# Kernel optimization log

Measured on AMD Instinct MI355X. Metric: run time of the kernel, lower is better.

## Reference

```python
import jax, jax.numpy as jnp
import numpy as np

# ---- module hyperparameters (init_kwargs) ----
V0 = 1.0
SIGMA0 = 0.5
GAUSS_CONST = V0 / (np.sqrt(2.0 * np.pi) * SIGMA0)
NW, NF, D, H = 4096, 16, 3, 256  # walkers, fermions, dimensions, hidden width
N = NF * D


def setup_inputs() -> dict:
    key = jax.random.key(0)
    k0, k1, k2, k3 = jax.random.split(key, 4)
    sc = lambda k, shape, fan_in: jax.random.normal(k, shape, jnp.float32) / np.sqrt(fan_in).astype(np.float32)
    return {
        "x": jax.random.normal(k0, (NW, NF, D), jnp.float32),
        "W1": sc(k1, (N, H), N),
        "b1": jnp.zeros((H,), jnp.float32),
        "W2": sc(k2, (H, H), H),
        "b2": jnp.zeros((H,), jnp.float32),
        "w3": sc(k3, (H,), H),
        "b3": jnp.zeros((), jnp.float32),
    }


def _logpsi(xf, W1, b1, W2, b2, w3, b3):
    # xf: (N,) flattened single-walker coordinates -> scalar log|psi|
    h = jnp.tanh(xf @ W1 + b1)
    h = jnp.tanh(h @ W2 + b2)
    return h @ w3 + b3


def reference(x, W1, b1, W2, b2, w3, b3):
    nw, nf, d = x.shape
    xflat = x.reshape(nw, nf * d)

    f = lambda xf: _logpsi(xf, W1, b1, W2, b2, w3, b3)
    grad_f = jax.grad(f)

    def kinetic_one(xf):
        g = grad_f(xf)                      # (N,) d logpsi / dx
        hess = jax.jacfwd(grad_f)(xf)       # (N, N) forward-over-reverse Hessian
        lap = jnp.trace(hess)
        return -0.5 * (lap + jnp.sum(g * g))

    kin = jax.vmap(kinetic_one)(xflat)      # (nw,)

    # harmonic potential 1/2 sum x^2
    pot = 0.5 * jnp.sum(xflat * xflat, axis=1)

    # Gaussian interaction, faithful to source: unsqueeze(-2)/unsqueeze(-1) on
    # (nw, nf, d) broadcasts to (nw, nf, d, d) intra-particle coordinate diffs,
    # then sum over last axis -> (nw, nf, d), triu(k=1) over trailing (nf, d).
    diff = x[..., None, :] - x[..., :, None]            # (nw, nf, d, d)
    sqdist = jnp.sum(diff * diff, axis=-1)              # (nw, nf, d)
    mask = jnp.triu(jnp.ones((nf, d), x.dtype), k=1)    # (nf, d)
    inter = GAUSS_CONST * jnp.sum(jnp.exp(-sqdist / (2.0 * SIGMA0 ** 2)) * mask, axis=(-2, -1))

    eloc = kin + pot + inter
    return (eloc, kin, pot, inter)
```

## Files before the change

kernel.cpp:

```cpp
#include <hip/hip_runtime.h>
#include <cmath>

#define NWALK 4096
#define NXD   48
#define HID   256
#define WPB   8
#define GCONST 0.7978845608028654f

typedef _Float16 half8   __attribute__((ext_vector_type(8)));
typedef float    float4v __attribute__((ext_vector_type(4)));

__global__ __launch_bounds__(256) void prep_all(const float* __restrict__ W2,
                                                const float* __restrict__ W1,
                                                const float* __restrict__ x,
                                                const float* __restrict__ b1,
                                                _Float16* __restrict__ W2c,
                                                _Float16* __restrict__ W1c,
                                                _Float16* __restrict__ t1h,
                                                _Float16* __restrict__ h1h,
                                                _Float16* __restrict__ ch) {
    __shared__ float tile[64][65];
    __shared__ float xs[16][NXD];

    if (blockIdx.x < 16) {
        const int bi = blockIdx.x & 3;
        const int bj = blockIdx.x >> 2;
        const int tx = threadIdx.x & 63;
        const int ty = threadIdx.x >> 6;
        #pragma unroll
        for (int r = 0; r < 16; ++r) {
            int il = ty * 16 + r;
            tile[tx][il] = W2[(bi * 64 + il) * HID + bj * 64 + tx];
        }
        __syncthreads();
        #pragma unroll
        for (int r = 0; r < 16; ++r) {
            int jl = ty * 16 + r;
            W2c[(bj * 64 + jl) * HID + bi * 64 + tx] = (_Float16)tile[jl][tx];
        }
        #pragma unroll
        for (int r = 0; r < 3; ++r) {
            int k = blockIdx.x * 3 + r;
            W1c[k * HID + threadIdx.x] = (_Float16)W1[k * HID + threadIdx.x];
        }
    } else {
        const int i  = threadIdx.x;
        const int w0 = (blockIdx.x - 16) * 16;

        float col[NXD];
        float S = 0.f;
        #pragma unroll
        for (int k = 0; k < NXD; ++k) {
            float v = W1[k * HID + i];
            col[k] = v;
            S = fmaf(v, v, S);
        }
        #pragma unroll
        for (int t = threadIdx.x; t < 16 * NXD; t += 256)
            ((float*)xs)[t] = x[w0 * NXD + t];
        __syncthreads();

        const float b = b1[i];
        #pragma unroll 4
        for (int w = 0; w < 16; ++w) {
            float a1 = b;
            #pragma unroll
            for (int k = 0; k < NXD; ++k)
                a1 = fmaf(xs[w][k], col[k], a1);
            float h1 = tanhf(a1);
            float t1 = 1.f - h1 * h1;
            int off = (w0 + w) * HID + i;
            t1h[off] = (_Float16)t1;
            h1h[off] = (_Float16)h1;
            ch[off]  = (_Float16)(S * h1 * t1);
        }
    }
}

__global__ __launch_bounds__(256, 2) void eloc8(
    const float* __restrict__ x,
    const float* __restrict__ b2,
    const float* __restrict__ w3,
    const _Float16* __restrict__ W2c,
    const _Float16* __restrict__ W1c,
    const _Float16* __restrict__ t1h,
    const _Float16* __restrict__ h1h,
    const _Float16* __restrict__ ch,
    float* __restrict__ out)
{
    __shared__ __align__(16) _Float16 AsT[48 * HID];
    __shared__ float xs[WPB][NXD];
    __shared__ float gw[WPB][4][NXD];
    __shared__ float rt1p[WPB][4][16];
    __shared__ float us[WPB][HID], uhs[WPB][HID];
    __shared__ float b2s[HID], w3s[HID];
    __shared__ float r2s[4][WPB];
    __shared__ float rt2s[WPB];

    const int w0   = blockIdx.x * WPB;
    const int tid  = threadIdx.x;
    const int wave = tid >> 6;
    const int lane = tid & 63;
    const int n16  = lane & 15;
    const int quad = (tid >> 4) & 3;
    const int ci   = tid & 31;
    const int k0   = tid >> 5;

    half8 afr[8][4];
    #pragma unroll
    for (int s = 0; s < 8; ++s)
        #pragma unroll
        for (int a = 0; a < 4; ++a)
            afr[s][a] = *(const half8*)(W2c + ((wave * 4 + a) * 16 + n16) * HID
                                        + s * 32 + quad * 8);

    b2s[tid] = b2[tid];
    w3s[tid] = w3[tid];
    #pragma unroll
    for (int t = tid; t < WPB * NXD; t += 256)
        ((float*)xs)[t] = x[w0 * NXD + t];

    {
        const _Float16* src  = (n16 & 1) ? ch : h1h;
        const _Float16* brow = src + (size_t)(w0 + (n16 >> 1)) * HID;

        float4v acc[4];
        #pragma unroll
        for (int a = 0; a < 4; ++a) acc[a] = (float4v){0.f, 0.f, 0.f, 0.f};
        #pragma unroll
        for (int s = 0; s < 8; ++s) {
            half8 bf = *(const half8*)(brow + (s * 4 + quad) * 8);
            #pragma unroll
            for (int a = 0; a < 4; ++a)
                acc[a] = __builtin_amdgcn_mfma_f32_16x16x32_f16(afr[s][a], bf, acc[a], 0, 0, 0);
        }

        {
            half8 th0 = *(const half8*)(t1h + (size_t)w0 * HID + ci * 8);
            #pragma unroll
            for (int s2 = 0; s2 < 6; ++s2) {
                int k = s2 * 8 + k0;
                half8 wv = *(const half8*)(W1c + k * HID + ci * 8);
                *(half8*)(AsT + k * HID + ((ci ^ (k & 7)) * 8)) = wv * th0;
            }
        }

        __syncthreads();

        const int w = n16 >> 1;
        float um[4][4];
        #pragma unroll
        for (int a = 0; a < 4; ++a)
            #pragma unroll
            for (int reg = 0; reg < 4; ++reg) um[a][reg] = 0.f;

        if (!(n16 & 1)) {
            #pragma unroll
            for (int a = 0; a < 4; ++a)
                #pragma unroll
                for (int reg = 0; reg < 4; ++reg) {
                    int i    = (wave * 4 + a) * 16 + quad * 4 + reg;
                    float a2 = acc[a][reg] + b2s[i];
                    float h2 = tanhf(a2);
                    float t2 = 1.f - h2 * h2;
                    float u  = w3s[i] * t2;
                    um[a][reg] = u;
                    us [w][i] = u;
                    uhs[w][i] = u * h2;
                }
        }

        float part = 0.f;
        #pragma unroll
        for (int a = 0; a < 4; ++a)
            #pragma unroll
            for (int reg = 0; reg < 4; ++reg) {
                float uo = __shfl_xor(um[a][reg], 1, 64);
                part = fmaf(uo, acc[a][reg], part);
            }
        part += __shfl_xor(part, 16, 64);
        part += __shfl_xor(part, 32, 64);
        if (quad == 0 && (n16 & 1)) r2s[wave][w] = part;
    }
    __syncthreads();
    if (tid < WPB)
        rt2s[tid] = r2s[0][tid] + r2s[1][tid] + r2s[2][tid] + r2s[3][tid];
    __syncthreads();

    #pragma unroll 1
    for (int ww = 0; ww < WPB; ++ww) {
        const int wg    = w0 + ww;
        const bool more = (ww + 1 < WPB);
        const int wn    = more ? (wg + 1) : wg;

        float4v uu[4];
        #pragma unroll
        for (int a = 0; a < 4; ++a)
            uu[a] = *(const float4v*)(&us[ww][(wave * 4 + a) * 16 + quad * 4]);

        float4v sq[4];
        #pragma unroll
        for (int a = 0; a < 4; ++a) sq[a] = (float4v){0.f, 0.f, 0.f, 0.f};

        #pragma unroll 1
        for (int kt = 0; kt < 3; ++kt) {
            const int krow = kt * 16 + n16;

            half8 bfv[8];
            #pragma unroll
            for (int s = 0; s < 8; ++s)
                bfv[s] = *(const half8*)(AsT + krow * HID
                          + ((((s * 4 + quad) ^ (krow & 7)) << 3)));

            float4v acc[4];
            #pragma unroll
            for (int a = 0; a < 4; ++a) acc[a] = (float4v){0.f, 0.f, 0.f, 0.f};

            __builtin_amdgcn_s_setprio(1);
            #pragma unroll
            for (int s = 0; s < 8; ++s)
                #pragma unroll
                for (int a = 0; a < 4; ++a)
                    acc[a] = __builtin_amdgcn_mfma_f32_16x16x32_f16(
                        afr[s][a], bfv[s], acc[a], 0, 0, 0);
            __builtin_amdgcn_s_setprio(0);

            float g = 0.f;
            #pragma unroll
            for (int a = 0; a < 4; ++a)
                #pragma unroll
                for (int reg = 0; reg < 4; ++reg) {
                    float m = acc[a][reg];
                    sq[a][reg] = fmaf(m, m, sq[a][reg]);
                    g          = fmaf(m, uu[a][reg], g);
                }
            g += __shfl_xor(g, 16, 64);
            g += __shfl_xor(g, 32, 64);
            if (lane < 16) gw[ww][wave][kt * 16 + lane] = g;
        }

        half8 th = *(const half8*)(t1h + (size_t)wn * HID + ci * 8);
        half8 w1v[6];
        #pragma unroll
        for (int s2 = 0; s2 < 6; ++s2)
            w1v[s2] = *(const half8*)(W1c + (s2 * 8 + k0) * HID + ci * 8);

        float rt1 = 0.f;
        #pragma unroll
        for (int a = 0; a < 4; ++a) {
            float4v uh = *(const float4v*)(&uhs[ww][(wave * 4 + a) * 16 + quad * 4]);
            #pragma unroll
            for (int reg = 0; reg < 4; ++reg)
                rt1 = fmaf(sq[a][reg], uh[reg], rt1);
        }
        rt1 += __shfl_xor(rt1, 16, 64);
        rt1 += __shfl_xor(rt1, 32, 64);
        if (lane < 16) rt1p[ww][wave][lane] = rt1;

        __syncthreads();

        if (more) {
            #pragma unroll
            for (int s2 = 0; s2 < 6; ++s2) {
                int k = s2 * 8 + k0;
                *(half8*)(AsT + k * HID + ((ci ^ (k & 7)) * 8)) = w1v[s2] * th;
            }
        }
        __syncthreads();
    }

    const int wa = 2 * wave, wb = wa + 1;
    float rt2a = rt2s[wa];
    float rt2b = rt2s[wb];

    float r0 = rt1p[wa][quad][n16];
    float r1 = rt1p[wb][quad][n16];

    float ga = 0.f, gb = 0.f, xa = 0.f, xb = 0.f;
    if (lane < NXD) {
        ga = gw[wa][0][lane] + gw[wa][1][lane] + gw[wa][2][lane] + gw[wa][3][lane];
        gb = gw[wb][0][lane] + gw[wb][1][lane] + gw[wb][2][lane] + gw[wb][3][lane];
        xa = xs[wa][lane];
        xb = xs[wb][lane];
    }
    float gga = ga * ga, ggb = gb * gb;
    float pa = 0.5f * xa * xa, pb = 0.5f * xb * xb;
    #pragma unroll
    for (int off = 32; off > 0; off >>= 1) {
        r0  += __shfl_down(r0,  off, 64);
        r1  += __shfl_down(r1,  off, 64);
        gga += __shfl_down(gga, off, 64);
        ggb += __shfl_down(ggb, off, 64);
        pa  += __shfl_down(pa,  off, 64);
        pb  += __shfl_down(pb,  off, 64);
    }
    if (lane == 0) {
        float kina = r0 + rt2a - 0.5f * gga;
        float kinb = r1 + rt2b - 0.5f * ggb;

        float x0 = xs[wa][0], x1 = xs[wa][1], x2 = xs[wa][2];
        float x3 = xs[wa][3], x4 = xs[wa][4], x5 = xs[wa][5];
        float d01 = (x0-x1)*(x0-x1) + (x2-x1)*(x2-x1);
        float d02 = (x0-x2)*(x0-x2) + (x1-x2)*(x1-x2);
        float d12 = (x3-x5)*(x3-x5) + (x4-x5)*(x4-x5);
        float intera = GCONST * (expf(-2.f*d01) + expf(-2.f*d02) + expf(-2.f*d12));

        x0 = xs[wb][0]; x1 = xs[wb][1]; x2 = xs[wb][2];
        x3 = xs[wb][3]; x4 = xs[wb][4]; x5 = xs[wb][5];
        float e01 = (x0-x1)*(x0-x1) + (x2-x1)*(x2-x1);
        float e02 = (x0-x2)*(x0-x2) + (x1-x2)*(x1-x2);
        float e12 = (x3-x5)*(x3-x5) + (x4-x5)*(x4-x5);
        float interb = GCONST * (expf(-2.f*e01) + expf(-2.f*e02) + expf(-2.f*e12));

        const int wga = w0 + wa, wgb = w0 + wb;
        out[wga]             = kina + pa + intera;
        out[NWALK + wga]     = kina;
        out[2 * NWALK + wga] = pa;
        out[3 * NWALK + wga] = intera;
        out[wgb]             = kinb + pb + interb;
        out[NWALK + wgb]     = kinb;
        out[2 * NWALK + wgb] = pb;
        out[3 * NWALK + wgb] = interb;
    }
}

extern "C" void kernel_launch(void* const* d_in, const int* in_sizes, int n_in,
                              void* d_out, int out_size, void* d_ws, size_t ws_size,
                              hipStream_t stream) {
    const float* x  = (const float*)d_in[0];
    const float* W1 = (const float*)d_in[1];
    const float* b1 = (const float*)d_in[2];
    const float* W2 = (const float*)d_in[3];
    const float* b2 = (const float*)d_in[4];
    const float* w3 = (const float*)d_in[5];
    float* out = (float*)d_out;

    char* ws = (char*)d_ws;
    _Float16* W2c = (_Float16*)(ws);
    _Float16* W1c = (_Float16*)(ws + 131072);
    _Float16* t1h = (_Float16*)(ws + 155648);
    _Float16* h1h = (_Float16*)(ws + 2252800);
    _Float16* chv = (_Float16*)(ws + 4349952);

    prep_all<<<16 + NWALK / 16, 256, 0, stream>>>(W2, W1, x, b1, W2c, W1c, t1h, h1h, chv);
    eloc8<<<NWALK / WPB, 256, 0, stream>>>(x, b2, w3, W2c, W1c, t1h, h1h, chv, out);
}
```

Baseline: 109.4 us.

## Split eloc8 across eight waves with half the W2 fragments each

Doubles the eloc8 block to 512 threads (8 waves). Each wave now holds only two 16-row slices of W2 in registers instead of four, which cuts register pressure and raises launch-bound occupancy. The B-fragment loads from LDS are split into two halves interleaved with the MFMA batches, and the next walker's t1 load is hoisted to the top of the loop. Cross-wave reductions and the final output stage are widened to cover eight partial sums, and each wave now finalizes one walker instead of two. The cost is more block-wide synchronisation and reduction traffic per walker.

```diff
diff --git a/kernel.cpp b/kernel.cpp
--- a/kernel.cpp
+++ b/kernel.cpp
@@ -77,7 +77,7 @@
     }
 }
 
-__global__ __launch_bounds__(256, 2) void eloc8(
+__global__ __launch_bounds__(512, 4) void eloc8(
     const float* __restrict__ x,
     const float* __restrict__ b2,
     const float* __restrict__ w3,
@@ -90,11 +90,11 @@
 {
     __shared__ __align__(16) _Float16 AsT[48 * HID];
     __shared__ float xs[WPB][NXD];
-    __shared__ float gw[WPB][4][NXD];
-    __shared__ float rt1p[WPB][4][16];
+    __shared__ float gw[WPB][8][NXD];
+    __shared__ float rt1p[WPB][8][16];
     __shared__ float us[WPB][HID], uhs[WPB][HID];
     __shared__ float b2s[HID], w3s[HID];
-    __shared__ float r2s[4][WPB];
+    __shared__ float r2s[8][WPB];
     __shared__ float rt2s[WPB];
 
     const int w0   = blockIdx.x * WPB;
@@ -102,44 +102,45 @@
     const int wave = tid >> 6;
     const int lane = tid & 63;
     const int n16  = lane & 15;
-    const int quad = (tid >> 4) & 3;
+    const int quad = lane >> 4;
     const int ci   = tid & 31;
     const int k0   = tid >> 5;
 
-    half8 afr[8][4];
+    half8 afr[8][2];
     #pragma unroll
     for (int s = 0; s < 8; ++s)
         #pragma unroll
-        for (int a = 0; a < 4; ++a)
-            afr[s][a] = *(const half8*)(W2c + ((wave * 4 + a) * 16 + n16) * HID
+        for (int a = 0; a < 2; ++a)
+            afr[s][a] = *(const half8*)(W2c + ((wave * 2 + a) * 16 + n16) * HID
                                         + s * 32 + quad * 8);
 
-    b2s[tid] = b2[tid];
-    w3s[tid] = w3[tid];
-    #pragma unroll
-    for (int t = tid; t < WPB * NXD; t += 256)
-        ((float*)xs)[t] = x[w0 * NXD + t];
+    if (tid < HID) {
+        b2s[tid] = b2[tid];
+        w3s[tid] = w3[tid];
+    }
+    if (tid < WPB * NXD)
+        ((float*)xs)[tid] = x[w0 * NXD + tid];
 
     {
         const _Float16* src  = (n16 & 1) ? ch : h1h;
         const _Float16* brow = src + (size_t)(w0 + (n16 >> 1)) * HID;
 
-        float4v acc[4];
-        #pragma unroll
-        for (int a = 0; a < 4; ++a) acc[a] = (float4v){0.f, 0.f, 0.f, 0.f};
+        float4v acc[2];
+        #pragma unroll
+        for (int a = 0; a < 2; ++a) acc[a] = (float4v){0.f, 0.f, 0.f, 0.f};
         #pragma unroll
         for (int s = 0; s < 8; ++s) {
             half8 bf = *(const half8*)(brow + (s * 4 + quad) * 8);
             #pragma unroll
-            for (int a = 0; a < 4; ++a)
+            for (int a = 0; a < 2; ++a)
                 acc[a] = __builtin_amdgcn_mfma_f32_16x16x32_f16(afr[s][a], bf, acc[a], 0, 0, 0);
         }
 
         {
             half8 th0 = *(const half8*)(t1h + (size_t)w0 * HID + ci * 8);
             #pragma unroll
-            for (int s2 = 0; s2 < 6; ++s2) {
-                int k = s2 * 8 + k0;
+            for (int s2 = 0; s2 < 3; ++s2) {
+                int k = s2 * 16 + k0;
                 half8 wv = *(const half8*)(W1c + k * HID + ci * 8);
                 *(half8*)(AsT + k * HID + ((ci ^ (k & 7)) * 8)) = wv * th0;
             }
@@ -148,18 +149,18 @@
         __syncthreads();
 
         const int w = n16 >> 1;
-        float um[4][4];
-        #pragma unroll
-        for (int a = 0; a < 4; ++a)
+        float um[2][4];
+        #pragma unroll
+        for (int a = 0; a < 2; ++a)
             #pragma unroll
             for (int reg = 0; reg < 4; ++reg) um[a][reg] = 0.f;
 
         if (!(n16 & 1)) {
             #pragma unroll
-            for (int a = 0; a < 4; ++a)
+            for (int a = 0; a < 2; ++a)
                 #pragma unroll
                 for (int reg = 0; reg < 4; ++reg) {
-                    int i    = (wave * 4 + a) * 16 + quad * 4 + reg;
+                    int i    = (wave * 2 + a) * 16 + quad * 4 + reg;
                     float a2 = acc[a][reg] + b2s[i];
                     float h2 = tanhf(a2);
                     float t2 = 1.f - h2 * h2;
@@ -172,7 +173,7 @@
 
         float part = 0.f;
         #pragma unroll
-        for (int a = 0; a < 4; ++a)
+        for (int a = 0; a < 2; ++a)
             #pragma unroll
             for (int reg = 0; reg < 4; ++reg) {
                 float uo = __shfl_xor(um[a][reg], 1, 64);
@@ -183,8 +184,12 @@
         if (quad == 0 && (n16 & 1)) r2s[wave][w] = part;
     }
     __syncthreads();
-    if (tid < WPB)
-        rt2s[tid] = r2s[0][tid] + r2s[1][tid] + r2s[2][tid] + r2s[3][tid];
+    if (tid < WPB) {
+        float s = 0.f;
+        #pragma unroll
+        for (int wv = 0; wv < 8; ++wv) s += r2s[wv][tid];
+        rt2s[tid] = s;
+    }
     __syncthreads();
 
     #pragma unroll 1
@@ -193,41 +198,54 @@
         const bool more = (ww + 1 < WPB);
         const int wn    = more ? (wg + 1) : wg;
 
-        float4v uu[4];
-        #pragma unroll
-        for (int a = 0; a < 4; ++a)
-            uu[a] = *(const float4v*)(&us[ww][(wave * 4 + a) * 16 + quad * 4]);
-
-        float4v sq[4];
-        #pragma unroll
-        for (int a = 0; a < 4; ++a) sq[a] = (float4v){0.f, 0.f, 0.f, 0.f};
+        half8 th = *(const half8*)(t1h + (size_t)wn * HID + ci * 8);
+
+        float4v uu[2];
+        #pragma unroll
+        for (int a = 0; a < 2; ++a)
+            uu[a] = *(const float4v*)(&us[ww][(wave * 2 + a) * 16 + quad * 4]);
+
+        float4v sq[2];
+        #pragma unroll
+        for (int a = 0; a < 2; ++a) sq[a] = (float4v){0.f, 0.f, 0.f, 0.f};
 
         #pragma unroll 1
         for (int kt = 0; kt < 3; ++kt) {
             const int krow = kt * 16 + n16;
 
-            half8 bfv[8];
-            #pragma unroll
-            for (int s = 0; s < 8; ++s)
+            float4v acc[2];
+            #pragma unroll
+            for (int a = 0; a < 2; ++a) acc[a] = (float4v){0.f, 0.f, 0.f, 0.f};
+
+            half8 bfv[4];
+            #pragma unroll
+            for (int s = 0; s < 4; ++s)
                 bfv[s] = *(const half8*)(AsT + krow * HID
                           + ((((s * 4 + quad) ^ (krow & 7)) << 3)));
-
-            float4v acc[4];
-            #pragma unroll
-            for (int a = 0; a < 4; ++a) acc[a] = (float4v){0.f, 0.f, 0.f, 0.f};
-
             __builtin_amdgcn_s_setprio(1);
             #pragma unroll
-            for (int s = 0; s < 8; ++s)
+            for (int s = 0; s < 4; ++s)
                 #pragma unroll
-                for (int a = 0; a < 4; ++a)
+                for (int a = 0; a < 2; ++a)
                     acc[a] = __builtin_amdgcn_mfma_f32_16x16x32_f16(
                         afr[s][a], bfv[s], acc[a], 0, 0, 0);
             __builtin_amdgcn_s_setprio(0);
+            #pragma unroll
+            for (int s = 0; s < 4; ++s)
+                bfv[s] = *(const half8*)(AsT + krow * HID
+                          + (((((s + 4) * 4 + quad) ^ (krow & 7)) << 3)));
+            __builtin_amdgcn_s_setprio(1);
+            #pragma unroll
+            for (int s = 0; s < 4; ++s)
+                #pragma unroll
+                for (int a = 0; a < 2; ++a)
+                    acc[a] = __builtin_amdgcn_mfma_f32_16x16x32_f16(
+                        afr[s + 4][a], bfv[s], acc[a], 0, 0, 0);
+            __builtin_amdgcn_s_setprio(0);
 
             float g = 0.f;
             #pragma unroll
-            for (int a = 0; a < 4; ++a)
+            for (int a = 0; a < 2; ++a)
                 #pragma unroll
                 for (int reg = 0; reg < 4; ++reg) {
                     float m = acc[a][reg];
@@ -239,16 +257,15 @@
             if (lane < 16) gw[ww][wave][kt * 16 + lane] = g;
         }
 
-        half8 th = *(const half8*)(t1h + (size_t)wn * HID + ci * 8);
-        half8 w1v[6];
-        #pragma unroll
-        for (int s2 = 0; s2 < 6; ++s2)
-            w1v[s2] = *(const half8*)(W1c + (s2 * 8 + k0) * HID + ci * 8);
+        half8 w1v[3];
+        #pragma unroll
+        for (int s2 = 0; s2 < 3; ++s2)
+            w1v[s2] = *(const half8*)(W1c + (s2 * 16 + k0) * HID + ci * 8);
 
         float rt1 = 0.f;
         #pragma unroll
-        for (int a = 0; a < 4; ++a) {
-            float4v uh = *(const float4v*)(&uhs[ww][(wave * 4 + a) * 16 + quad * 4]);
+        for (int a = 0; a < 2; ++a) {
+            float4v uh = *(const float4v*)(&uhs[ww][(wave * 2 + a) * 16 + quad * 4]);
             #pragma unroll
             for (int reg = 0; reg < 4; ++reg)
                 rt1 = fmaf(sq[a][reg], uh[reg], rt1);
@@ -261,42 +278,36 @@
 
         if (more) {
             #pragma unroll
-            for (int s2 = 0; s2 < 6; ++s2) {
-                int k = s2 * 8 + k0;
+            for (int s2 = 0; s2 < 3; ++s2) {
+                int k = s2 * 16 + k0;
                 *(half8*)(AsT + k * HID + ((ci ^ (k & 7)) * 8)) = w1v[s2] * th;
             }
         }
         __syncthreads();
     }
 
-    const int wa = 2 * wave, wb = wa + 1;
+    const int wa = wave;
     float rt2a = rt2s[wa];
-    float rt2b = rt2s[wb];
-
-    float r0 = rt1p[wa][quad][n16];
-    float r1 = rt1p[wb][quad][n16];
-
-    float ga = 0.f, gb = 0.f, xa = 0.f, xb = 0.f;
+
+    const int p4 = lane >> 4;
+    float r0 = rt1p[wa][p4][n16] + rt1p[wa][p4 + 4][n16];
+
+    float ga = 0.f, xa = 0.f;
     if (lane < NXD) {
-        ga = gw[wa][0][lane] + gw[wa][1][lane] + gw[wa][2][lane] + gw[wa][3][lane];
-        gb = gw[wb][0][lane] + gw[wb][1][lane] + gw[wb][2][lane] + gw[wb][3][lane];
+        #pragma unroll
+        for (int wv = 0; wv < 8; ++wv) ga += gw[wa][wv][lane];
         xa = xs[wa][lane];
-        xb = xs[wb][lane];
-    }
-    float gga = ga * ga, ggb = gb * gb;
-    float pa = 0.5f * xa * xa, pb = 0.5f * xb * xb;
+    }
+    float gga = ga * ga;
+    float pa  = 0.5f * xa * xa;
     #pragma unroll
     for (int off = 32; off > 0; off >>= 1) {
         r0  += __shfl_down(r0,  off, 64);
-        r1  += __shfl_down(r1,  off, 64);
         gga += __shfl_down(gga, off, 64);
-        ggb += __shfl_down(ggb, off, 64);
         pa  += __shfl_down(pa,  off, 64);
-        pb  += __shfl_down(pb,  off, 64);
     }
     if (lane == 0) {
         float kina = r0 + rt2a - 0.5f * gga;
-        float kinb = r1 + rt2b - 0.5f * ggb;
 
         float x0 = xs[wa][0], x1 = xs[wa][1], x2 = xs[wa][2];
         float x3 = xs[wa][3], x4 = xs[wa][4], x5 = xs[wa][5];
@@ -305,22 +316,11 @@
         float d12 = (x3-x5)*(x3-x5) + (x4-x5)*(x4-x5);
         float intera = GCONST * (expf(-2.f*d01) + expf(-2.f*d02) + expf(-2.f*d12));
 
-        x0 = xs[wb][0]; x1 = xs[wb][1]; x2 = xs[wb][2];
-        x3 = xs[wb][3]; x4 = xs[wb][4]; x5 = xs[wb][5];
-        float e01 = (x0-x1)*(x0-x1) + (x2-x1)*(x2-x1);
-        float e02 = (x0-x2)*(x0-x2) + (x1-x2)*(x1-x2);
-        float e12 = (x3-x5)*(x3-x5) + (x4-x5)*(x4-x5);
-        float interb = GCONST * (expf(-2.f*e01) + expf(-2.f*e02) + expf(-2.f*e12));
-
-        const int wga = w0 + wa, wgb = w0 + wb;
+        const int wga = w0 + wa;
         out[wga]             = kina + pa + intera;
         out[NWALK + wga]     = kina;
         out[2 * NWALK + wga] = pa;
         out[3 * NWALK + wga] = intera;
-        out[wgb]             = kinb + pb + interb;
-        out[NWALK + wgb]     = kinb;
-        out[2 * NWALK + wgb] = pb;
-        out[3 * NWALK + wgb] = interb;
     }
 }
 
@@ -343,5 +343,5 @@
     _Float16* chv = (_Float16*)(ws + 4349952);
 
     prep_all<<<16 + NWALK / 16, 256, 0, stream>>>(W2, W1, x, b1, W2c, W1c, t1h, h1h, chv);
-    eloc8<<<NWALK / WPB, 256, 0, stream>>>(x, b2, w3, W2c, W1c, t1h, h1h, chv, out);
+    eloc8<<<NWALK / WPB, 512, 0, stream>>>(x, b2, w3, W2c, W1c, t1h, h1h, chv, out);
 }
```

Measured after the change: 122.8 us. 1.12x slower.

## Form scaled W1 operand in registers, drop shared staging and per-walker barriers

Applied to the files above, without the earlier changes.

Stops staging the per-walker W1·diag(t1) product in shared memory. Each wave now loads W1 rows and t1 fragments directly from global memory (L2-resident) and multiplies them in registers just before the MFMAs. This removes the 24 KB LDS buffer and the two block-wide barriers per walker. The cost is redundant global loads and packed fp16 multiplies in every wave, plus global load latency inside the inner k-loop.

```diff
diff --git a/kernel.cpp b/kernel.cpp
--- a/kernel.cpp
+++ b/kernel.cpp
@@ -88,7 +88,6 @@
     const _Float16* __restrict__ ch,
     float* __restrict__ out)
 {
-    __shared__ __align__(16) _Float16 AsT[48 * HID];
     __shared__ float xs[WPB][NXD];
     __shared__ float gw[WPB][4][NXD];
     __shared__ float rt1p[WPB][4][16];
@@ -103,8 +102,6 @@
     const int lane = tid & 63;
     const int n16  = lane & 15;
     const int quad = (tid >> 4) & 3;
-    const int ci   = tid & 31;
-    const int k0   = tid >> 5;
 
     half8 afr[8][4];
     #pragma unroll
@@ -133,16 +130,6 @@
             #pragma unroll
             for (int a = 0; a < 4; ++a)
                 acc[a] = __builtin_amdgcn_mfma_f32_16x16x32_f16(afr[s][a], bf, acc[a], 0, 0, 0);
-        }
-
-        {
-            half8 th0 = *(const half8*)(t1h + (size_t)w0 * HID + ci * 8);
-            #pragma unroll
-            for (int s2 = 0; s2 < 6; ++s2) {
-                int k = s2 * 8 + k0;
-                half8 wv = *(const half8*)(W1c + k * HID + ci * 8);
-                *(half8*)(AsT + k * HID + ((ci ^ (k & 7)) * 8)) = wv * th0;
-            }
         }
 
         __syncthreads();
@@ -189,9 +176,12 @@
 
     #pragma unroll 1
     for (int ww = 0; ww < WPB; ++ww) {
-        const int wg    = w0 + ww;
-        const bool more = (ww + 1 < WPB);
-        const int wn    = more ? (wg + 1) : wg;
+        const int wg = w0 + ww;
+
+        half8 t1f[8];
+        #pragma unroll
+        for (int s = 0; s < 8; ++s)
+            t1f[s] = *(const half8*)(t1h + (size_t)wg * HID + (s * 4 + quad) * 8);
 
         float4v uu[4];
         #pragma unroll
@@ -205,12 +195,12 @@
         #pragma unroll 1
         for (int kt = 0; kt < 3; ++kt) {
             const int krow = kt * 16 + n16;
-
-            half8 bfv[8];
+            const _Float16* wrow = W1c + krow * HID;
+
+            half8 w1v[8];
             #pragma unroll
             for (int s = 0; s < 8; ++s)
-                bfv[s] = *(const half8*)(AsT + krow * HID
-                          + ((((s * 4 + quad) ^ (krow & 7)) << 3)));
+                w1v[s] = *(const half8*)(wrow + (s * 4 + quad) * 8);
 
             float4v acc[4];
             #pragma unroll
@@ -218,11 +208,13 @@
 
             __builtin_amdgcn_s_setprio(1);
             #pragma unroll
-            for (int s = 0; s < 8; ++s)
+            for (int s = 0; s < 8; ++s) {
+                half8 bf = w1v[s] * t1f[s];
                 #pragma unroll
                 for (int a = 0; a < 4; ++a)
                     acc[a] = __builtin_amdgcn_mfma_f32_16x16x32_f16(
-                        afr[s][a], bfv[s], acc[a], 0, 0, 0);
+                        afr[s][a], bf, acc[a], 0, 0, 0);
+            }
             __builtin_amdgcn_s_setprio(0);
 
             float g = 0.f;
@@ -239,12 +231,6 @@
             if (lane < 16) gw[ww][wave][kt * 16 + lane] = g;
         }
 
-        half8 th = *(const half8*)(t1h + (size_t)wn * HID + ci * 8);
-        half8 w1v[6];
-        #pragma unroll
-        for (int s2 = 0; s2 < 6; ++s2)
-            w1v[s2] = *(const half8*)(W1c + (s2 * 8 + k0) * HID + ci * 8);
-
         float rt1 = 0.f;
         #pragma unroll
         for (int a = 0; a < 4; ++a) {
@@ -256,18 +242,9 @@
         rt1 += __shfl_xor(rt1, 16, 64);
         rt1 += __shfl_xor(rt1, 32, 64);
         if (lane < 16) rt1p[ww][wave][lane] = rt1;
-
-        __syncthreads();
-
-        if (more) {
-            #pragma unroll
-            for (int s2 = 0; s2 < 6; ++s2) {
-                int k = s2 * 8 + k0;
-                *(half8*)(AsT + k * HID + ((ci ^ (k & 7)) * 8)) = w1v[s2] * th;
-            }
-        }
-        __syncthreads();
-    }
+    }
+
+    __syncthreads();
 
     const int wa = 2 * wave, wb = wa + 1;
     float rt2a = rt2s[wa];
```

Result: slower. 134.0 us (+22.6%).
